# Optimization experiments

Hardware: AMD Instinct MI355X
Metric: run time of the kernel (lower is better)

## Reference

```python
import jax, jax.numpy as jnp
import numpy as np
from jax import lax


def build_scharr_filter(size):
    assert size % 2 == 1
    c = size // 2
    wx = np.zeros((size, size), np.float32)
    wy = np.zeros((size, size), np.float32)
    for i in range(size):
        for j in range(size):
            dx = j - c
            dy = i - c
            wx[i, j] = dx * (3 if abs(dx) == 1 else 10 if dx == 0 else 1)
            wy[i, j] = dy * (3 if abs(dy) == 1 else 10 if dy == 0 else 1)
    return jnp.asarray(wx), jnp.asarray(wy)


SIZE = 3


def build_normals(xyz, size=SIZE):
    # xyz: (B, 3, H, W). Depthwise conv: for each of x,y,z apply scharr_x and scharr_y.
    kx, ky = build_scharr_filter(size)
    # kernel (6,1,s,s): [Sxx, Sxy, Syx, Syy, Szx, Szy] via feature_group_count=3
    kernel = jnp.stack([kx, ky, kx, ky, kx, ky])[:, None]
    p = size // 2
    g = lax.conv_general_dilated(
        xyz, kernel, window_strides=(1, 1), padding=[(p, p), (p, p)],
        dimension_numbers=("NCHW", "OIHW", "NCHW"), feature_group_count=3)
    Sxx, Sxy = g[:, 0:1], g[:, 1:2]
    Syx, Syy = g[:, 2:3], g[:, 3:4]
    Szx, Szy = g[:, 4:5], g[:, 5:6]
    normal = jnp.concatenate([
        Syx * Szy - Szx * Syy,
        Szx * Sxy - Szy * Sxx,
        Sxx * Syy - Syx * Sxy,
    ], axis=1)
    n = jnp.linalg.norm(normal, axis=1, keepdims=True) + jnp.float32(1e-10)
    return normal / n


def setup_inputs() -> dict:
    key = jax.random.key(0)
    k1, k2, k3 = jax.random.split(key, 3)
    B, H, W = 16, 384, 1280
    xyz_pred = jax.random.normal(k1, (B, 3, H, W), dtype=jnp.float32)
    xyz_gt = jax.random.normal(k2, (B, 3, H, W), dtype=jnp.float32)
    mask = jax.random.uniform(k3, (B, 1, H, W), dtype=jnp.float32)
    return {"xyz_pred": xyz_pred, "xyz_gt": xyz_gt, "mask": mask}


def reference(xyz_pred, xyz_gt, mask):
    normals_pred = build_normals(xyz_pred)
    normals_gt = build_normals(xyz_gt)
    loss = jnp.sum(mask * jnp.abs(normals_pred - normals_gt))
    denom = jnp.sum(mask)
    return loss / denom
```

## Files before the change

### kernel.cpp

```cpp
#include <hip/hip_runtime.h>

#define BB  16
#define HH  384
#define WW  1280
#define TPB 256
#define ROWS 16
#define NSLOT 64

__device__ __forceinline__ void load_row3(const float* __restrict__ plane, int i, int j,
                                          float& a, float& b, float& c) {
    const float* row = plane + (size_t)i * WW;
    a = (j > 0)      ? row[j - 1] : 0.f;
    b = row[j];
    c = (j < WW - 1) ? row[j + 1] : 0.f;
}

__global__ __launch_bounds__(TPB)
void NormalLoss_44478681317469_main(const float* __restrict__ pred,
                                    const float* __restrict__ gt,
                                    const float* __restrict__ mask,
                                    double* __restrict__ acc)
{
    const int j  = blockIdx.x * TPB + threadIdx.x;
    const int r0 = blockIdx.y * ROWS;
    const int b  = blockIdx.z;

    const float* pl[6];
#pragma unroll
    for (int c = 0; c < 3; ++c) {
        pl[c]     = pred + (size_t)(b * 3 + c) * HH * WW;
        pl[3 + c] = gt   + (size_t)(b * 3 + c) * HH * WW;
    }
    const float* mpl = mask + (size_t)b * HH * WW;

    float Dm1[6], D0[6], Dp1[6], Tm1[6], T0[6], Tp1[6];
    float Ra[6], Rb[6], Rc[6];

#pragma unroll
    for (int c = 0; c < 6; ++c) {
        if (r0 > 0) {
            float a, bb, cc; load_row3(pl[c], r0 - 1, j, a, bb, cc);
            Dm1[c] = cc - a; Tm1[c] = a + bb + cc;
        } else { Dm1[c] = 0.f; Tm1[c] = 0.f; }
        {
            float a, bb, cc; load_row3(pl[c], r0, j, a, bb, cc);
            D0[c] = cc - a; T0[c] = a + bb + cc;
        }
    }

#pragma unroll
    for (int c = 0; c < 6; ++c) {
        if (r0 + 1 < HH) load_row3(pl[c], r0 + 1, j, Ra[c], Rb[c], Rc[c]);
        else             { Ra[c] = 0.f; Rb[c] = 0.f; Rc[c] = 0.f; }
    }
    float mrow = mpl[(size_t)r0 * WW + j];

    float lsum = 0.f, msum = 0.f;

#pragma unroll
    for (int k = 0; k < ROWS; ++k) {
        const int i = r0 + k;

#pragma unroll
        for (int c = 0; c < 6; ++c) {
            Dp1[c] = Rc[c] - Ra[c];
            Tp1[c] = Ra[c] + Rb[c] + Rc[c];
        }
        float m = mrow;

        if (i + 2 < HH) {
#pragma unroll
            for (int c = 0; c < 6; ++c) load_row3(pl[c], i + 2, j, Ra[c], Rb[c], Rc[c]);
        } else {
#pragma unroll
            for (int c = 0; c < 6; ++c) { Ra[c] = 0.f; Rb[c] = 0.f; Rc[c] = 0.f; }
        }
        if (k + 1 < ROWS) mrow = mpl[(size_t)(i + 1) * WW + j];

        float gx[6], gy[6];
#pragma unroll
        for (int c = 0; c < 6; ++c) {
            gx[c] = Dm1[c] + D0[c] + Dp1[c];
            gy[c] = Tp1[c] - Tm1[c];
        }

        float n0p = gx[1] * gy[2] - gx[2] * gy[1];
        float n1p = gx[2] * gy[0] - gx[0] * gy[2];
        float n2p = gx[0] * gy[1] - gx[1] * gy[0];
        float n0g = gx[4] * gy[5] - gx[5] * gy[4];
        float n1g = gx[5] * gy[3] - gx[3] * gy[5];
        float n2g = gx[3] * gy[4] - gx[4] * gy[3];

        float sp = n0p * n0p + n1p * n1p + n2p * n2p;
        float sg = n0g * n0g + n1g * n1g + n2g * n2g;
        float ip = (sp > 1e-20f) ? __builtin_amdgcn_rsqf(sp) : 0.f;
        float ig = (sg > 1e-20f) ? __builtin_amdgcn_rsqf(sg) : 0.f;

        float d0 = fabsf(n0p * ip - n0g * ig);
        float d1 = fabsf(n1p * ip - n1g * ig);
        float d2 = fabsf(n2p * ip - n2g * ig);

        lsum += m * (d0 + d1 + d2);
        msum += m;

#pragma unroll
        for (int c = 0; c < 6; ++c) {
            Dm1[c] = D0[c]; D0[c] = Dp1[c];
            Tm1[c] = T0[c]; T0[c] = Tp1[c];
        }
    }

#pragma unroll
    for (int off = 32; off > 0; off >>= 1) {
        lsum += __shfl_down(lsum, off, 64);
        msum += __shfl_down(msum, off, 64);
    }
    __shared__ float sL[TPB / 64], sM[TPB / 64];
    const int lane = threadIdx.x & 63;
    const int wid  = threadIdx.x >> 6;
    if (lane == 0) { sL[wid] = lsum; sM[wid] = msum; }
    __syncthreads();
    if (threadIdx.x == 0) {
        float L = 0.f, M = 0.f;
#pragma unroll
        for (int w = 0; w < TPB / 64; ++w) { L += sL[w]; M += sM[w]; }
        const int linear = (blockIdx.z * gridDim.y + blockIdx.y) * gridDim.x + blockIdx.x;
        double* slot = acc + (size_t)(linear & (NSLOT - 1)) * 8;
        atomicAdd(&slot[0], (double)L);
        atomicAdd(&slot[1], (double)M);
    }
}

__global__ void NormalLoss_44478681317469_final(const double* __restrict__ acc,
                                                float* __restrict__ out)
{
    const int t = threadIdx.x;
    double L = acc[(size_t)t * 8 + 0];
    double M = acc[(size_t)t * 8 + 1];
#pragma unroll
    for (int off = 32; off > 0; off >>= 1) {
        L += __shfl_down(L, off, 64);
        M += __shfl_down(M, off, 64);
    }
    if (t == 0) out[0] = (float)(L / M);
}

extern "C" void kernel_launch(void* const* d_in, const int* in_sizes, int n_in,
                              void* d_out, int out_size, void* d_ws, size_t ws_size,
                              hipStream_t stream)
{
    const float* pred = (const float*)d_in[0];
    const float* gt   = (const float*)d_in[1];
    const float* mask = (const float*)d_in[2];
    double* acc = (double*)d_ws;

    hipMemsetAsync(acc, 0, NSLOT * 8 * sizeof(double), stream);

    dim3 grid(WW / TPB, HH / ROWS, BB);
    NormalLoss_44478681317469_main<<<grid, dim3(TPB), 0, stream>>>(pred, gt, mask, acc);
    NormalLoss_44478681317469_final<<<1, 64, 0, stream>>>(acc, (float*)d_out);
}
```

Measured before the change: 270.6 us.

## Vectorize columns to float4 per thread with single-wave blocks

```diff
diff --git a/kernel.cpp b/kernel.cpp
--- a/kernel.cpp
+++ b/kernel.cpp
@@ -3,27 +3,40 @@
 #define BB  16
 #define HH  384
 #define WW  1280
-#define TPB 256
-#define ROWS 16
+#define TPB 64
+#define ROWS 8
 #define NSLOT 64
 
-__device__ __forceinline__ void load_row3(const float* __restrict__ plane, int i, int j,
-                                          float& a, float& b, float& c) {
-    const float* row = plane + (size_t)i * WW;
-    a = (j > 0)      ? row[j - 1] : 0.f;
-    b = row[j];
-    c = (j < WW - 1) ? row[j + 1] : 0.f;
-}
-
-__global__ __launch_bounds__(TPB)
+__device__ __forceinline__ float4 f4add(const float4 a, const float4 b) {
+    return make_float4(a.x + b.x, a.y + b.y, a.z + b.z, a.w + b.w);
+}
+__device__ __forceinline__ float4 f4sub(const float4 a, const float4 b) {
+    return make_float4(a.x - b.x, a.y - b.y, a.z - b.z, a.w - b.w);
+}
+__device__ __forceinline__ float getc(const float4& v, int k) {
+    return k == 0 ? v.x : k == 1 ? v.y : k == 2 ? v.z : v.w;
+}
+
+__device__ __forceinline__ void DT(float el, const float4 q, float er,
+                                   bool hl, bool hr, float4& D, float4& T) {
+    float lv = hl ? el : 0.f;
+    float rv = hr ? er : 0.f;
+    D.x = q.y - lv;       T.x = lv + q.x + q.y;
+    D.y = q.z - q.x;      T.y = q.x + q.y + q.z;
+    D.z = q.w - q.y;      T.z = q.y + q.z + q.w;
+    D.w = rv - q.z;       T.w = q.z + q.w + rv;
+}
+
+__global__ __launch_bounds__(TPB, 3)
 void NormalLoss_44478681317469_main(const float* __restrict__ pred,
                                     const float* __restrict__ gt,
                                     const float* __restrict__ mask,
                                     double* __restrict__ acc)
 {
-    const int j  = blockIdx.x * TPB + threadIdx.x;
-    const int r0 = blockIdx.y * ROWS;
-    const int b  = blockIdx.z;
+    const int lane = threadIdx.x;
+    const int col0 = blockIdx.x * 256 + lane * 4;
+    const int r0   = blockIdx.y * ROWS;
+    const int b    = blockIdx.z;
 
     const float* pl[6];
 #pragma unroll
@@ -33,27 +46,43 @@
     }
     const float* mpl = mask + (size_t)b * HH * WW;
 
-    float Dm1[6], D0[6], Dp1[6], Tm1[6], T0[6], Tp1[6];
-    float Ra[6], Rb[6], Rc[6];
-
-#pragma unroll
-    for (int c = 0; c < 6; ++c) {
-        if (r0 > 0) {
-            float a, bb, cc; load_row3(pl[c], r0 - 1, j, a, bb, cc);
-            Dm1[c] = cc - a; Tm1[c] = a + bb + cc;
-        } else { Dm1[c] = 0.f; Tm1[c] = 0.f; }
-        {
-            float a, bb, cc; load_row3(pl[c], r0, j, a, bb, cc);
-            D0[c] = cc - a; T0[c] = a + bb + cc;
-        }
-    }
-
-#pragma unroll
-    for (int c = 0; c < 6; ++c) {
-        if (r0 + 1 < HH) load_row3(pl[c], r0 + 1, j, Ra[c], Rb[c], Rc[c]);
-        else             { Ra[c] = 0.f; Rb[c] = 0.f; Rc[c] = 0.f; }
-    }
-    float mrow = mpl[(size_t)r0 * WW + j];
+    const bool has_l = (col0 > 0);
+    const bool has_r = (col0 + 4 < WW);
+    const int  jl    = has_l ? col0 - 1 : 0;
+    const int  jr    = has_r ? col0 + 4 : WW - 1;
+
+    float4 A[6], D0[6], Tm1[6], T0[6];
+    float4 Q[6]; float EL[6], ER[6];
+    float4 mrow;
+
+    {
+        const int rb0 = r0 * WW;
+#pragma unroll
+        for (int c = 0; c < 6; ++c) {
+            float4 Dm1c = make_float4(0.f, 0.f, 0.f, 0.f);
+            Tm1[c] = make_float4(0.f, 0.f, 0.f, 0.f);
+            if (r0 > 0) {
+                const int rbm = (r0 - 1) * WW;
+                float4 q = *(const float4*)(pl[c] + rbm + col0);
+                float el = pl[c][rbm + jl], er = pl[c][rbm + jr];
+                DT(el, q, er, has_l, has_r, Dm1c, Tm1[c]);
+            }
+            {
+                float4 q = *(const float4*)(pl[c] + rb0 + col0);
+                float el = pl[c][rb0 + jl], er = pl[c][rb0 + jr];
+                DT(el, q, er, has_l, has_r, D0[c], T0[c]);
+            }
+            A[c] = f4add(Dm1c, D0[c]);
+        }
+        const int rb1 = (r0 + 1) * WW;
+#pragma unroll
+        for (int c = 0; c < 6; ++c) {
+            Q[c]  = *(const float4*)(pl[c] + rb1 + col0);
+            EL[c] = pl[c][rb1 + jl];
+            ER[c] = pl[c][rb1 + jr];
+        }
+        mrow = *(const float4*)(mpl + rb0 + col0);
+    }
 
     float lsum = 0.f, msum = 0.f;
 
@@ -61,52 +90,69 @@
     for (int k = 0; k < ROWS; ++k) {
         const int i = r0 + k;
 
-#pragma unroll
-        for (int c = 0; c < 6; ++c) {
-            Dp1[c] = Rc[c] - Ra[c];
-            Tp1[c] = Ra[c] + Rb[c] + Rc[c];
-        }
-        float m = mrow;
+        float4 Dp1[6], Tp1[6];
+#pragma unroll
+        for (int c = 0; c < 6; ++c)
+            DT(EL[c], Q[c], ER[c], has_l, has_r, Dp1[c], Tp1[c]);
+        const float4 m = mrow;
 
         if (i + 2 < HH) {
-#pragma unroll
-            for (int c = 0; c < 6; ++c) load_row3(pl[c], i + 2, j, Ra[c], Rb[c], Rc[c]);
+            const int rb = (i + 2) * WW;
+#pragma unroll
+            for (int c = 0; c < 6; ++c) {
+                Q[c]  = *(const float4*)(pl[c] + rb + col0);
+                EL[c] = pl[c][rb + jl];
+                ER[c] = pl[c][rb + jr];
+            }
         } else {
 #pragma unroll
-            for (int c = 0; c < 6; ++c) { Ra[c] = 0.f; Rb[c] = 0.f; Rc[c] = 0.f; }
-        }
-        if (k + 1 < ROWS) mrow = mpl[(size_t)(i + 1) * WW + j];
-
-        float gx[6], gy[6];
-#pragma unroll
-        for (int c = 0; c < 6; ++c) {
-            gx[c] = Dm1[c] + D0[c] + Dp1[c];
-            gy[c] = Tp1[c] - Tm1[c];
-        }
-
-        float n0p = gx[1] * gy[2] - gx[2] * gy[1];
-        float n1p = gx[2] * gy[0] - gx[0] * gy[2];
-        float n2p = gx[0] * gy[1] - gx[1] * gy[0];
-        float n0g = gx[4] * gy[5] - gx[5] * gy[4];
-        float n1g = gx[5] * gy[3] - gx[3] * gy[5];
-        float n2g = gx[3] * gy[4] - gx[4] * gy[3];
-
-        float sp = n0p * n0p + n1p * n1p + n2p * n2p;
-        float sg = n0g * n0g + n1g * n1g + n2g * n2g;
-        float ip = (sp > 1e-20f) ? __builtin_amdgcn_rsqf(sp) : 0.f;
-        float ig = (sg > 1e-20f) ? __builtin_amdgcn_rsqf(sg) : 0.f;
-
-        float d0 = fabsf(n0p * ip - n0g * ig);
-        float d1 = fabsf(n1p * ip - n1g * ig);
-        float d2 = fabsf(n2p * ip - n2g * ig);
-
-        lsum += m * (d0 + d1 + d2);
-        msum += m;
-
-#pragma unroll
-        for (int c = 0; c < 6; ++c) {
-            Dm1[c] = D0[c]; D0[c] = Dp1[c];
-            Tm1[c] = T0[c]; T0[c] = Tp1[c];
+            for (int c = 0; c < 6; ++c) {
+                Q[c] = make_float4(0.f, 0.f, 0.f, 0.f); EL[c] = 0.f; ER[c] = 0.f;
+            }
+        }
+        if (k + 1 < ROWS) mrow = *(const float4*)(mpl + (i + 1) * WW + col0);
+
+        float4 gx[6], gy[6];
+#pragma unroll
+        for (int c = 0; c < 6; ++c) {
+            gx[c] = f4add(A[c], Dp1[c]);
+            gy[c] = f4sub(Tp1[c], Tm1[c]);
+        }
+
+#pragma unroll
+        for (int p = 0; p < 4; ++p) {
+            float gx0 = getc(gx[0], p), gx1 = getc(gx[1], p), gx2 = getc(gx[2], p);
+            float gy0 = getc(gy[0], p), gy1 = getc(gy[1], p), gy2 = getc(gy[2], p);
+            float hx0 = getc(gx[3], p), hx1 = getc(gx[4], p), hx2 = getc(gx[5], p);
+            float hy0 = getc(gy[3], p), hy1 = getc(gy[4], p), hy2 = getc(gy[5], p);
+
+            float n0p = gx1 * gy2 - gx2 * gy1;
+            float n1p = gx2 * gy0 - gx0 * gy2;
+            float n2p = gx0 * gy1 - gx1 * gy0;
+            float n0g = hx1 * hy2 - hx2 * hy1;
+            float n1g = hx2 * hy0 - hx0 * hy2;
+            float n2g = hx0 * hy1 - hx1 * hy0;
+
+            float sp = n0p * n0p + n1p * n1p + n2p * n2p;
+            float sg = n0g * n0g + n1g * n1g + n2g * n2g;
+            float ip = (sp > 1e-20f) ? __builtin_amdgcn_rsqf(sp) : 0.f;
+            float ig = (sg > 1e-20f) ? __builtin_amdgcn_rsqf(sg) : 0.f;
+
+            float d0 = fabsf(n0p * ip - n0g * ig);
+            float d1 = fabsf(n1p * ip - n1g * ig);
+            float d2 = fabsf(n2p * ip - n2g * ig);
+
+            float mv = getc(m, p);
+            lsum += mv * (d0 + d1 + d2);
+            msum += mv;
+        }
+
+#pragma unroll
+        for (int c = 0; c < 6; ++c) {
+            A[c]   = f4add(D0[c], Dp1[c]);
+            D0[c]  = Dp1[c];
+            Tm1[c] = T0[c];
+            T0[c]  = Tp1[c];
         }
     }
 
@@ -115,19 +161,11 @@
         lsum += __shfl_down(lsum, off, 64);
         msum += __shfl_down(msum, off, 64);
     }
-    __shared__ float sL[TPB / 64], sM[TPB / 64];
-    const int lane = threadIdx.x & 63;
-    const int wid  = threadIdx.x >> 6;
-    if (lane == 0) { sL[wid] = lsum; sM[wid] = msum; }
-    __syncthreads();
-    if (threadIdx.x == 0) {
-        float L = 0.f, M = 0.f;
-#pragma unroll
-        for (int w = 0; w < TPB / 64; ++w) { L += sL[w]; M += sM[w]; }
+    if (lane == 0) {
         const int linear = (blockIdx.z * gridDim.y + blockIdx.y) * gridDim.x + blockIdx.x;
         double* slot = acc + (size_t)(linear & (NSLOT - 1)) * 8;
-        atomicAdd(&slot[0], (double)L);
-        atomicAdd(&slot[1], (double)M);
+        atomicAdd(&slot[0], (double)lsum);
+        atomicAdd(&slot[1], (double)msum);
     }
 }
 
@@ -156,7 +194,7 @@
 
     hipMemsetAsync(acc, 0, NSLOT * 8 * sizeof(double), stream);
 
-    dim3 grid(WW / TPB, HH / ROWS, BB);
+    dim3 grid(WW / 256, HH / ROWS, BB);
     NormalLoss_44478681317469_main<<<grid, dim3(TPB), 0, stream>>>(pred, gt, mask, acc);
     NormalLoss_44478681317469_final<<<1, 64, 0, stream>>>(acc, (float*)d_out);
 }
```

Measured after the change: 481.8 us. 1.78x slower.
